# Optimization experiments

Measured on AMD Instinct MI355X. Metric: run time of the kernel, lower is better.

Reference implementation:

```python
import jax, jax.numpy as jnp
import numpy as np

MAX_M = 16
B, H, N_LEN = 16, 256, 4096


def _ref_dft_np(n, h):
    a = np.arange(n)
    M = np.exp(-2j * np.pi * np.outer(a, a) / n)  # (n, n) complex
    M = np.broadcast_to(M, (h, n, n))
    return np.ascontiguousarray(np.stack([M.real, M.imag], axis=-1)).astype(np.float32)


def setup_inputs() -> dict:
    key = jax.random.key(0)
    k1, k2 = jax.random.split(key)
    x_real = jax.random.normal(k1, (B, H, N_LEN), dtype=jnp.float32)
    x_imag = jax.random.normal(k2, (B, H, N_LEN), dtype=jnp.float32)
    # Learned DFT matrices are initialized to the exact reference DFT matrices
    # (learn_additive=False path in the torch module).
    return {
        "x_real": x_real,
        "x_imag": x_imag,
        "mat_2": jnp.asarray(_ref_dft_np(2, H)),
        "mat_4": jnp.asarray(_ref_dft_np(4, H)),
        "mat_8": jnp.asarray(_ref_dft_np(8, H)),
        "mat_16": jnp.asarray(_ref_dft_np(16, H)),
        "N": N_LEN,
    }


def _twiddle(n, m):
    na = jnp.arange(n)[:, None]
    ma = jnp.arange(m)[None, :]
    return jnp.exp((-2j * jnp.pi / (n * m)) * (na * ma).astype(jnp.float32))  # (n, m)


def _cooley_tukey(k, n, m, mats):
    # k: (..., n*m) complex; FFT of length n*m along last dim.
    k = k.reshape(k.shape[:-1] + (m, n))  # '... (m n) -> ... m n'
    # n m-length DFTs along rows: mats[m] is (H, m, m), broadcasts over leading dims.
    k_f = jnp.einsum('...mo,...on->...mn', mats[m], k)
    twi = _twiddle(n, m).astype(k_f.dtype)  # (n, m)
    k_f = jnp.einsum('nm,...mn->...nm', twi, k_f)  # transpose + twiddle
    if n <= MAX_M:
        k_f = jnp.einsum('...no,...om->...nm', mats[n], k_f)
    else:
        k_f = jnp.moveaxis(k_f, -1, -3)  # '... h n m -> ... m h n'
        k_f = _cooley_tukey(k_f, n // MAX_M, MAX_M, mats)
        k_f = jnp.moveaxis(k_f, -3, -1)  # '... m h n -> ... h n m'
    return k_f.reshape(k_f.shape[:-2] + (k_f.shape[-2] * k_f.shape[-1],))


def reference(x_real, x_imag, mat_2, mat_4, mat_8, mat_16, N):
    x = x_real + 1j * x_imag  # (B, H, N) complex64
    mats = {p: (mm[..., 0] + 1j * mm[..., 1])
            for p, mm in ((2, mat_2), (4, mat_4), (8, mat_8), (16, mat_16))}
    out = _cooley_tukey(x, N // MAX_M, MAX_M, mats)  # (B, H, N) complex
    # view_as_real representation of the complex FFT output
    return jnp.stack([out.real, out.imag], axis=-1)  # (B, H, N, 2)
```

## Files before the change

### kernel.cpp

```cpp
#include <hip/hip_runtime.h>
#include <stdint.h>

typedef _Float16 f16x8 __attribute__((ext_vector_type(8)));
typedef float    f32x4 __attribute__((ext_vector_type(4)));

union FragU { unsigned u[4]; f16x8 h; };
union H2U  { unsigned u; _Float16 h[2]; };

__device__ __forceinline__ unsigned pkh(float a, float b) {
    return __builtin_bit_cast(unsigned, __builtin_amdgcn_cvt_pkrtz(a, b));
}
__device__ __forceinline__ unsigned short h16(float a) {
    return __builtin_bit_cast(unsigned short, (_Float16)a);
}

#define MFMA(A, B, C) __builtin_amdgcn_mfma_f32_16x16x32_f16((A).h, (B).h, (C), 0, 0, 0)

#define K1 (-1.5339807878856412e-03f)
#define K2 (-2.4543692606170259e-02f)

__global__ __launch_bounds__(256, 6) void fft4096_mfma(
    const float* __restrict__ xre, const float* __restrict__ xim,
    const float* __restrict__ mat16, float* __restrict__ out, int H)
{
    __shared__ __align__(16) unsigned char smem[32768];

    const int t = threadIdx.x;
    const int w = t >> 6;
    const int l = t & 63;
    const int g = l >> 4;
    const int c = l & 15;
    const int bh = blockIdx.x;
    const int h  = bh % H;
    const size_t base = (size_t)bh * 4096;

    float xr[4][4], xi[4][4];
#pragma unroll
    for (int p = 0; p < 4; ++p) {
        const int col = (4 * w + p) * 16 + c;
#pragma unroll
        for (int jj = 0; jj < 4; ++jj) {
            xr[p][jj] = xre[base + (size_t)((4 * g + jj) * 256 + col)];
            xi[p][jj] = xim[base + (size_t)((4 * g + jj) * 256 + col)];
        }
    }

    const float* Mb = mat16 + (size_t)h * 512 + (size_t)c * 32 + g * 8;
    const float4 mf0 = *(const float4*)Mb;
    const float4 mf1 = *(const float4*)(Mb + 4);
    const unsigned mrA = pkh(mf0.x, mf0.z), mrB = pkh(mf1.x, mf1.z);
    const unsigned miA = pkh(mf0.y, mf0.w), miB = pkh(mf1.y, mf1.w);
    const unsigned nmiA = miA ^ 0x80008000u, nmiB = miB ^ 0x80008000u;

    FragU Afrag;
    Afrag.u[0] = mrA; Afrag.u[1] = mrB; Afrag.u[2] = miA; Afrag.u[3] = miB;
    FragU BMr;
    BMr.u[0] = mrA; BMr.u[1] = mrB; BMr.u[2] = nmiA; BMr.u[3] = nmiB;
    FragU BMi;
    BMi.u[0] = miA; BMi.u[1] = miB; BMi.u[2] = mrA; BMi.u[3] = mrB;

    const f32x4 zero = {0.f, 0.f, 0.f, 0.f};

    f32x4 s1r[4], s1i[4];
#pragma unroll
    for (int p = 0; p < 4; ++p) {
        const unsigned rp0 = pkh(xr[p][0], xr[p][1]), rp1 = pkh(xr[p][2], xr[p][3]);
        const unsigned ip0 = pkh(xi[p][0], xi[p][1]), ip1 = pkh(xi[p][2], xi[p][3]);
        const unsigned np0 = ip0 ^ 0x80008000u, np1 = ip1 ^ 0x80008000u;
        FragU Br; Br.u[0] = rp0; Br.u[1] = rp1; Br.u[2] = np0; Br.u[3] = np1;
        FragU Bi; Bi.u[0] = ip0; Bi.u[1] = ip1; Bi.u[2] = rp0; Bi.u[3] = rp1;
        s1r[p] = MFMA(Afrag, Br, zero);
        s1i[p] = MFMA(Afrag, Bi, zero);
    }
#pragma unroll
    for (int p = 0; p < 4; ++p) {
        const int j = (4 * w + p) * 16 + c;
        float sb, cb, ss, cs;
        __sincosf(K1 * (float)(j * 4 * g), &sb, &cb);
        __sincosf(K1 * (float)j, &ss, &cs);
#pragma unroll
        for (int reg = 0; reg < 4; ++reg) {
            const float yr = s1r[p][reg], yi = s1i[p][reg];
            s1r[p][reg] = yr * cb - yi * sb;
            s1i[p][reg] = yr * sb + yi * cb;
            const float nc = cb * cs - sb * ss;
            const float ns = cb * ss + sb * cs;
            cb = nc; sb = ns;
        }
    }
#pragma unroll
    for (int reg = 0; reg < 4; ++reg) {
        const int m1 = 4 * g + reg;
        const int half = m1 * 256 + c * 16 + 4 * ((w ^ (c >> 2) ^ reg) & 3);
        uint2 vr, vi;
        vr.x = pkh(s1r[0][reg], s1r[1][reg]); vr.y = pkh(s1r[2][reg], s1r[3][reg]);
        vi.x = pkh(s1i[0][reg], s1i[1][reg]); vi.y = pkh(s1i[2][reg], s1i[3][reg]);
        *(uint2*)(smem + half * 2)        = vr;
        *(uint2*)(smem + 8192 + half * 2) = vi;
    }
    __syncthreads();

    uint2 rp[4], ip[4];
#pragma unroll
    for (int p = 0; p < 4; ++p) {
        const int m1 = 4 * w + p;
        const int half = m1 * 256 + c * 16 + 4 * ((g ^ (c >> 2) ^ p) & 3);
        rp[p] = *(const uint2*)(smem + half * 2);
        ip[p] = *(const uint2*)(smem + 8192 + half * 2);
    }
    f32x4 s2r[4], s2i[4];
#pragma unroll
    for (int p = 0; p < 4; ++p) {
        FragU Br; Br.u[0] = rp[p].x; Br.u[1] = rp[p].y;
        Br.u[2] = ip[p].x ^ 0x80008000u; Br.u[3] = ip[p].y ^ 0x80008000u;
        FragU Bi; Bi.u[0] = ip[p].x; Bi.u[1] = ip[p].y; Bi.u[2] = rp[p].x; Bi.u[3] = rp[p].y;
        s2r[p] = MFMA(Afrag, Br, zero);
        s2i[p] = MFMA(Afrag, Bi, zero);
    }
    {
        float twc[4], tws[4];
        float sb, cb, ss, cs;
        __sincosf(K2 * (float)(c * 4 * g), &sb, &cb);
        __sincosf(K2 * (float)c, &ss, &cs);
#pragma unroll
        for (int reg = 0; reg < 4; ++reg) {
            twc[reg] = cb; tws[reg] = sb;
            const float nc = cb * cs - sb * ss;
            const float ns = cb * ss + sb * cs;
            cb = nc; sb = ns;
        }
#pragma unroll
        for (int p = 0; p < 4; ++p) {
#pragma unroll
            for (int reg = 0; reg < 4; ++reg) {
                const float yr = s2r[p][reg], yi = s2i[p][reg];
                s2r[p][reg] = yr * twc[reg] - yi * tws[reg];
                s2i[p][reg] = yr * tws[reg] + yi * twc[reg];
            }
        }
    }
#pragma unroll
    for (int reg = 0; reg < 4; ++reg) {
        const int m2 = 4 * g + reg;
#pragma unroll
        for (int p = 0; p < 4; ++p) {
            const int spos = (((4 * w + p) * 16 + c) ^ (g << 4)) ^ (reg << 2);
            const int half = m2 * 256 + spos;
            *(unsigned short*)(smem + 16384 + half * 2) = h16(s2r[p][reg]);
            *(unsigned short*)(smem + 24576 + half * 2) = h16(s2i[p][reg]);
        }
    }

    FragU Aup[4];
#pragma unroll
    for (int p = 0; p < 4; ++p) {
        const int spos = ((((4 * w + p) * 16 + 4 * g) ^ (((c >> 2) & 3) << 4))
                          ^ ((c & 3) << 2));
        const int half = c * 256 + spos;
        const uint2 hr = *(const uint2*)(smem + 16384 + half * 2);
        const uint2 hi = *(const uint2*)(smem + 24576 + half * 2);
        Aup[p].u[0] = hr.x; Aup[p].u[1] = hr.y;
        Aup[p].u[2] = hi.x; Aup[p].u[3] = hi.y;
    }
    __syncthreads();

    f32x4 vR[4], vI[4];
#pragma unroll
    for (int p = 0; p < 4; ++p) {
        vR[p] = MFMA(Aup[p], BMr, zero);
        vI[p] = MFMA(Aup[p], BMi, zero);
    }

    {
        const int key = (c & 7) ^ ((g & 1) << 3);
#pragma unroll
        for (int reg = 0; reg < 4; ++reg) {
            const int Pl = (4 * g + reg) * 8 + 2 * w;
            const int P0 = Pl ^ key, P1 = (Pl + 1) ^ key;
            uint2 v0, v1;
            v0.x = pkh(vR[0][reg], vI[0][reg]); v0.y = pkh(vR[1][reg], vI[1][reg]);
            v1.x = pkh(vR[2][reg], vI[2][reg]); v1.y = pkh(vR[3][reg], vI[3][reg]);
            *(uint2*)(smem + (size_t)(c * 256 + 2 * P0) * 4) = v0;
            *(uint2*)(smem + (size_t)(c * 256 + 2 * P1) * 4) = v1;
        }
    }
    __syncthreads();

    f32x4* __restrict__ og4 = (f32x4*)out;
    const int tl = t & 127;
#pragma unroll
    for (int it = 0; it < 8; ++it) {
        const int jr = 2 * it + (t >> 7);
        const int Ps = tl ^ (jr & 7) ^ (((tl >> 5) & 1) << 3);
        const uint2 pv = *(const uint2*)(smem + (size_t)(jr * 256 + 2 * Ps) * 4);
        H2U a, b; a.u = pv.x; b.u = pv.y;
        const f32x4 v = {(float)a.h[0], (float)a.h[1], (float)b.h[0], (float)b.h[1]};
        __builtin_nontemporal_store(v, &og4[(base >> 1) + (size_t)(jr * 128 + tl)]);
    }
}

extern "C" void kernel_launch(void* const* d_in, const int* in_sizes, int n_in,
                              void* d_out, int out_size, void* d_ws, size_t ws_size,
                              hipStream_t stream)
{
    const float* xre = (const float*)d_in[0];
    const float* xim = (const float*)d_in[1];
    const float* m16 = (const float*)d_in[5];
    const int H  = in_sizes[5] / 512;
    const int BH = in_sizes[0] / 4096;
    fft4096_mfma<<<dim3(BH), dim3(256), 0, stream>>>(
        xre, xim, m16, (float*)d_out, H);
}
```

Measured before the change: 46.72 us.

## Swap operand roles in final DFT stage and store results directly to global

The third DFT stage now uses the matrix as the A operand and the shared-memory data as the B operand, as the first two stages do. The MFMA accumulators therefore already hold output-ordered values. This removes the final shared-memory staging pass, one barrier, and the fp16 round-trip of the results, which are now written straight to global memory as float2 nontemporal stores. In exchange the global stores become 8-byte scattered writes rather than 16-byte coalesced rows, and the shared-memory swizzle for the second-stage writes is redesigned.

```diff
diff --git a/kernel.cpp b/kernel.cpp
--- a/kernel.cpp
+++ b/kernel.cpp
@@ -3,9 +3,9 @@
 
 typedef _Float16 f16x8 __attribute__((ext_vector_type(8)));
 typedef float    f32x4 __attribute__((ext_vector_type(4)));
+typedef float    f32x2 __attribute__((ext_vector_type(2)));
 
 union FragU { unsigned u[4]; f16x8 h; };
-union H2U  { unsigned u; _Float16 h[2]; };
 
 __device__ __forceinline__ unsigned pkh(float a, float b) {
     return __builtin_bit_cast(unsigned, __builtin_amdgcn_cvt_pkrtz(a, b));
@@ -48,16 +48,9 @@
     const float* Mb = mat16 + (size_t)h * 512 + (size_t)c * 32 + g * 8;
     const float4 mf0 = *(const float4*)Mb;
     const float4 mf1 = *(const float4*)(Mb + 4);
-    const unsigned mrA = pkh(mf0.x, mf0.z), mrB = pkh(mf1.x, mf1.z);
-    const unsigned miA = pkh(mf0.y, mf0.w), miB = pkh(mf1.y, mf1.w);
-    const unsigned nmiA = miA ^ 0x80008000u, nmiB = miB ^ 0x80008000u;
-
     FragU Afrag;
-    Afrag.u[0] = mrA; Afrag.u[1] = mrB; Afrag.u[2] = miA; Afrag.u[3] = miB;
-    FragU BMr;
-    BMr.u[0] = mrA; BMr.u[1] = mrB; BMr.u[2] = nmiA; BMr.u[3] = nmiB;
-    FragU BMi;
-    BMi.u[0] = miA; BMi.u[1] = miB; BMi.u[2] = mrA; BMi.u[3] = mrB;
+    Afrag.u[0] = pkh(mf0.x, mf0.z); Afrag.u[1] = pkh(mf1.x, mf1.z);
+    Afrag.u[2] = pkh(mf0.y, mf0.w); Afrag.u[3] = pkh(mf1.y, mf1.w);
 
     const f32x4 zero = {0.f, 0.f, 0.f, 0.f};
 
@@ -144,58 +137,33 @@
         const int m2 = 4 * g + reg;
 #pragma unroll
         for (int p = 0; p < 4; ++p) {
-            const int spos = (((4 * w + p) * 16 + c) ^ (g << 4)) ^ (reg << 2);
-            const int half = m2 * 256 + spos;
+            const int half = m2 * 256 + (4 * w + p) * 16
+                           + 4 * (((c >> 2) ^ p ^ w) & 3) + (c & 3);
             *(unsigned short*)(smem + 16384 + half * 2) = h16(s2r[p][reg]);
             *(unsigned short*)(smem + 24576 + half * 2) = h16(s2i[p][reg]);
         }
     }
+    __syncthreads();
 
-    FragU Aup[4];
+    float* __restrict__ og = out;
+    const int rslot = 4 * ((g ^ (c & 3) ^ (c >> 2)) & 3);
 #pragma unroll
     for (int p = 0; p < 4; ++p) {
-        const int spos = ((((4 * w + p) * 16 + 4 * g) ^ (((c >> 2) & 3) << 4))
-                          ^ ((c & 3) << 2));
-        const int half = c * 256 + spos;
+        const int m2 = 4 * w + p;
+        const int half = m2 * 256 + c * 16 + rslot;
         const uint2 hr = *(const uint2*)(smem + 16384 + half * 2);
         const uint2 hi = *(const uint2*)(smem + 24576 + half * 2);
-        Aup[p].u[0] = hr.x; Aup[p].u[1] = hr.y;
-        Aup[p].u[2] = hi.x; Aup[p].u[3] = hi.y;
-    }
-    __syncthreads();
-
-    f32x4 vR[4], vI[4];
-#pragma unroll
-    for (int p = 0; p < 4; ++p) {
-        vR[p] = MFMA(Aup[p], BMr, zero);
-        vI[p] = MFMA(Aup[p], BMi, zero);
-    }
-
-    {
-        const int key = (c & 7) ^ ((g & 1) << 3);
+        FragU Br; Br.u[0] = hr.x; Br.u[1] = hr.y;
+        Br.u[2] = hi.x ^ 0x80008000u; Br.u[3] = hi.y ^ 0x80008000u;
+        FragU Bi; Bi.u[0] = hi.x; Bi.u[1] = hi.y; Bi.u[2] = hr.x; Bi.u[3] = hr.y;
+        const f32x4 vr = MFMA(Afrag, Br, zero);
+        const f32x4 vi = MFMA(Afrag, Bi, zero);
 #pragma unroll
         for (int reg = 0; reg < 4; ++reg) {
-            const int Pl = (4 * g + reg) * 8 + 2 * w;
-            const int P0 = Pl ^ key, P1 = (Pl + 1) ^ key;
-            uint2 v0, v1;
-            v0.x = pkh(vR[0][reg], vI[0][reg]); v0.y = pkh(vR[1][reg], vI[1][reg]);
-            v1.x = pkh(vR[2][reg], vI[2][reg]); v1.y = pkh(vR[3][reg], vI[3][reg]);
-            *(uint2*)(smem + (size_t)(c * 256 + 2 * P0) * 4) = v0;
-            *(uint2*)(smem + (size_t)(c * 256 + 2 * P1) * 4) = v1;
+            const size_t k = base + (size_t)((4 * g + reg) * 256 + m2 * 16 + c);
+            const f32x2 v = {vr[reg], vi[reg]};
+            __builtin_nontemporal_store(v, (f32x2*)(og + 2 * k));
         }
-    }
-    __syncthreads();
-
-    f32x4* __restrict__ og4 = (f32x4*)out;
-    const int tl = t & 127;
-#pragma unroll
-    for (int it = 0; it < 8; ++it) {
-        const int jr = 2 * it + (t >> 7);
-        const int Ps = tl ^ (jr & 7) ^ (((tl >> 5) & 1) << 3);
-        const uint2 pv = *(const uint2*)(smem + (size_t)(jr * 256 + 2 * Ps) * 4);
-        H2U a, b; a.u = pv.x; b.u = pv.y;
-        const f32x4 v = {(float)a.h[0], (float)a.h[1], (float)b.h[0], (float)b.h[1]};
-        __builtin_nontemporal_store(v, &og4[(base >> 1) + (size_t)(jr * 128 + tl)]);
     }
 }
 
```

Result: no change. 47.07 us (+0.8%).
